# Performance work log

Measured on AMD Instinct MI355X. Metric: run time of the kernel, lower is better.

Reference implementation:

```python
import jax, jax.numpy as jnp
import numpy as np

GROUP = 32          # microscale group size for both acts and weights
FP8_MAX = 448.0     # float8_e4m3fn max
FP4_TABLE = jnp.array([0.0, 0.5, 1.0, 1.5, 2.0, 3.0, 4.0, 6.0,
                       -0.0, -0.5, -1.0, -1.5, -2.0, -3.0, -4.0, -6.0], dtype=jnp.float32)


def _ue8m0_to_float(sf):
    # uint8 exponent byte placed directly into the fp32 exponent field: 2^(e-127)
    return jax.lax.bitcast_convert_type(sf.astype(jnp.uint32) << 23, jnp.float32)


def _dequant_mxfp4(w_packed, sf):
    # w_packed: [..., K//2] ints in [0,256), two e2m1 nibbles per byte (low nibble = even elem)
    lo = FP4_TABLE[w_packed & 0xF]
    hi = FP4_TABLE[(w_packed >> 4) & 0xF]
    w = jnp.stack([lo, hi], axis=-1).reshape(*w_packed.shape[:-1], -1)   # [..., K]
    s = _ue8m0_to_float(sf)                                              # [..., K//32]
    w = w.reshape(*sf.shape, GROUP) * s[..., None]
    return w.reshape(*w_packed.shape[:-1], 2 * w_packed.shape[-1])


def _quant_dequant_fp8(x):
    # Faithful to _deepseek_v4_stage_mega_moe_inputs_kernel: per-32-group amax,
    # scale = amax/448 rounded UP to a power of two (UE8M0), cast to fp8 e4m3.
    T, D = x.shape
    xg = x.reshape(T, D // GROUP, GROUP)
    amax = jnp.maximum(jnp.max(jnp.abs(xg), axis=-1), 1e-4)
    scale = amax / FP8_MAX
    bits = jax.lax.bitcast_convert_type(scale, jnp.uint32)
    exp = ((bits >> 23) & 0xFF) + ((bits & 0x7FFFFF) != 0).astype(jnp.uint32)
    exp = jnp.clip(exp, 1, 254)
    rscale = jax.lax.bitcast_convert_type(exp << 23, jnp.float32)
    q = (xg * (1.0 / rscale)[..., None]).astype(jnp.float8_e4m3fn)
    return (q.astype(jnp.float32) * rscale[..., None]).reshape(T, D)


def setup_inputs() -> dict:
    key = jax.random.key(0)
    ks = jax.random.split(key, 7)
    T, D, I, E, K = 512, 2048, 768, 16, 8
    hidden_states = jax.random.normal(ks[0], (T, D), dtype=jnp.float32)
    topk_weights = jax.random.uniform(ks[1], (T, K), dtype=jnp.float32)
    topk_weights = topk_weights / jnp.sum(topk_weights, axis=-1, keepdims=True)
    topk_ids = jax.random.randint(ks[2], (T, K), 0, E, dtype=jnp.int32)
    w13_weight = jax.random.randint(ks[3], (E, 2 * I, D // 2), 0, 256, dtype=jnp.int32)
    w13_weight_scale = jax.random.randint(ks[4], (E, 2 * I, D // GROUP), 120, 128, dtype=jnp.int32)
    w2_weight = jax.random.randint(ks[5], (E, D, I // 2), 0, 256, dtype=jnp.int32)
    w2_weight_scale = jax.random.randint(ks[6], (E, D, I // GROUP), 120, 128, dtype=jnp.int32)
    return {"hidden_states": hidden_states, "topk_weights": topk_weights,
            "topk_ids": topk_ids, "w13_weight": w13_weight,
            "w13_weight_scale": w13_weight_scale, "w2_weight": w2_weight,
            "w2_weight_scale": w2_weight_scale}


def reference(hidden_states, topk_weights, topk_ids, w13_weight, w13_weight_scale,
              w2_weight, w2_weight_scale):
    E = w13_weight.shape[0]
    I = w13_weight.shape[1] // 2
    x = _quant_dequant_fp8(hidden_states)                 # [T, D] fp8-quantized acts
    w13 = _dequant_mxfp4(w13_weight, w13_weight_scale)    # [E, 2I, D]
    w2 = _dequant_mxfp4(w2_weight, w2_weight_scale)       # [E, D, I]
    onehot = (topk_ids[:, :, None] == jnp.arange(E)[None, None, :]).astype(jnp.float32)  # [T,K,E]
    routed = jnp.any(onehot > 0, axis=1)                  # [T, E]
    Xe = routed.T[:, :, None].astype(x.dtype) * x[None]   # [E, T, D]
    h = jnp.einsum('etd,efd->etf', Xe, w13)               # [E, T, 2I]
    gate, up = h[..., :I], h[..., I:]
    a = jax.nn.silu(gate) * up                            # SiluAndMul
    ye = jnp.einsum('eti,edi->etd', a, w2)                # [E, T, D]
    comb = jnp.einsum('tke,tk->te', onehot, topk_weights) # [T, E] routing weights
    return jnp.einsum('te,etd->td', comb, ye)             # [T, D]
```

## Files before the change

### kernel.cpp

```cpp
#include <hip/hip_runtime.h>
#include <stdint.h>
#include <math.h>

#define T_TOK 512
#define DDIM  2048
#define IDIM  768
#define NEXP  16
#define TOPK  8
#define LDB   72

typedef __attribute__((ext_vector_type(8))) short bf16x8;
typedef __attribute__((ext_vector_type(4))) float f32x4;

__device__ __forceinline__ float e4m3_rtne(float f) {
  uint32_t u = __float_as_uint(f);
  uint32_t sign = u & 0x80000000u;
  uint32_t a = u & 0x7FFFFFFFu;
  float fa = __uint_as_float(a);
  float out;
  if (fa >= 0.015625f) {
    uint32_t lsb = (a >> 20) & 1u;
    a += 0x0007FFFFu + lsb;
    a &= 0xFFF00000u;
    out = __uint_as_float(a);
  } else {
    out = rintf(fa * 512.0f) * 0.001953125f;
  }
  return __uint_as_float(__float_as_uint(out) | sign);
}

__global__ void qdq_kernel(const float* __restrict__ x, ushort* __restrict__ xq) {
  int idx = blockIdx.x * 256 + threadIdx.x;
  float v = x[idx];
  float a = fabsf(v);
#pragma unroll
  for (int m = 16; m >= 1; m >>= 1)
    a = fmaxf(a, __shfl_xor(a, m, 32));
  a = fmaxf(a, 1e-4f);
  float scale = a / 448.0f;
  uint32_t b = __float_as_uint(scale);
  uint32_t ex = ((b >> 23) & 255u) + ((b & 0x7FFFFFu) ? 1u : 0u);
  ex = ex < 1u ? 1u : (ex > 254u ? 254u : ex);
  float rscale = __uint_as_float(ex << 23);
  float inv = 1.0f / rscale;
  float r = e4m3_rtne(v * inv) * rscale;
  xq[idx] = (ushort)(__float_as_uint(r) >> 16);
}

__global__ void route_kernel(const int* __restrict__ ids, const float* __restrict__ wts,
                             int* counts, int* offsets, int* lists, float* combs,
                             int* tpe, int* tps, int* tpn) {
  int t = threadIdx.x;
  int  myid[TOPK];
  float myw[TOPK];
#pragma unroll
  for (int k = 0; k < TOPK; k++) { myid[k] = ids[t*TOPK+k]; myw[k] = wts[t*TOPK+k]; }
  int np = 0;
  for (int e = 0; e < NEXP; e++) {
    float s = 0.f; bool r = false;
#pragma unroll
    for (int k = 0; k < TOPK; k++) if (myid[k] == e) { s += myw[k]; r = true; }
    if (r) {
      int slot = atomicAdd(&counts[e], 1);
      lists[(e<<9) + slot] = t;
      combs[(e<<9) + slot] = s;
      tpe[t*TOPK + np] = e;
      tps[t*TOPK + np] = slot;
      np++;
    }
  }
  tpn[t] = np;
  __syncthreads();
  if (t == 0) {
    int acc = 0;
    for (int e = 0; e < NEXP; e++) {
      offsets[e] = acc;
      acc += atomicAdd(&counts[e], 0);
    }
    offsets[NEXP] = acc;
  }
}

__device__ __forceinline__ uint32_t dec2(uint32_t w8, uint32_t S) {
  uint32_t lo = w8 & 15u, hi = (w8 >> 4) & 15u;
  uint32_t mlo = lo & 7u, mhi = hi & 7u;
  uint32_t clo = (mlo < 2u) ? 0u : mlo;
  uint32_t chi = (mhi < 2u) ? 0u : mhi;
  uint32_t blo = (mlo == 0u) ? 0u : ((S + clo) << 6);
  uint32_t bhi = (mhi == 0u) ? 0u : ((S + chi) << 6);
  blo |= (lo & 8u) << 12;
  bhi |= (hi & 8u) << 12;
  return blo | (bhi << 16);
}

__global__ __launch_bounds__(128,2) void gemm1_kernel(
    const ushort* __restrict__ xq, const int* __restrict__ w13,
    const int* __restrict__ w13s, const int* __restrict__ counts,
    const int* __restrict__ offsets, const int* __restrict__ lists,
    const float* __restrict__ combs, ushort* __restrict__ a_buf)
{
  const int e  = blockIdx.x;
  const int i0 = blockIdx.y << 5;
  const int m0 = blockIdx.z << 7;
  const int cnt = counts[e];
  if (m0 >= cnt) return;

  __shared__ __align__(16) ushort Bsh[64*LDB];
  __shared__ int   toks[128];
  __shared__ float cmbs[128];

  const int tid = threadIdx.x;
  { int m = m0 + tid; bool v = m < cnt;
    toks[tid] = v ? lists[(e<<9)+m] : 0;
    cmbs[tid] = v ? combs[(e<<9)+m] : 0.f; }
  __syncthreads();

  const int wv = tid >> 6, l = tid & 63, l16 = l & 15, q = l >> 4;

  const ushort* arow[4];
#pragma unroll
  for (int i = 0; i < 4; i++) {
    int row = wv*64 + i*16 + l16;
    arow[i] = xq + (size_t)toks[row]*DDIM + q*8;
  }

  const int rb = tid >> 1, hb = tid & 1;
  const int feat = (rb < 32) ? (i0 + rb) : (IDIM + i0 + (rb - 32));
  const int* wrow = w13 + ((size_t)e*(2*IDIM) + feat)*(DDIM/2) + hb*16;
  const int* srow = w13s + ((size_t)e*(2*IDIM) + feat)*(DDIM/32);
  ushort* bdst = Bsh + rb*LDB + hb*32;

  f32x4 acc[4][4];
#pragma unroll
  for (int i = 0; i < 4; i++)
#pragma unroll
    for (int j = 0; j < 4; j++) acc[i][j] = (f32x4){0.f,0.f,0.f,0.f};

  for (int k0 = 0; k0 < DDIM; k0 += 64) {
    int4 wq[4];
    const int4* bp = (const int4*)(wrow + (k0 >> 1));
#pragma unroll
    for (int c = 0; c < 4; c++) wq[c] = bp[c];
    uint32_t S = (((uint32_t)srow[(k0 >> 5) + hb]) - 1u) << 1;

    bf16x8 afr[4][2];
#pragma unroll
    for (int i = 0; i < 4; i++)
#pragma unroll
      for (int s = 0; s < 2; s++)
        afr[i][s] = *(const bf16x8*)(arow[i] + k0 + s*32);

    __syncthreads();
    {
      uint32_t od[16];
      const int* wi = (const int*)wq;
#pragma unroll
      for (int c = 0; c < 16; c++) od[c] = dec2((uint32_t)wi[c], S);
#pragma unroll
      for (int c = 0; c < 4; c++)
        *(uint4*)(bdst + c*8) = make_uint4(od[4*c], od[4*c+1], od[4*c+2], od[4*c+3]);
    }
    __syncthreads();

#pragma unroll
    for (int s = 0; s < 2; s++) {
      bf16x8 bfr[4];
#pragma unroll
      for (int j = 0; j < 4; j++)
        bfr[j] = *(const bf16x8*)(Bsh + (j*16 + l16)*LDB + s*32 + q*8);
#pragma unroll
      for (int i = 0; i < 4; i++)
#pragma unroll
        for (int j = 0; j < 4; j++)
          acc[i][j] = __builtin_amdgcn_mfma_f32_16x16x32_bf16(afr[i][s], bfr[j], acc[i][j], 0, 0, 0);
    }
  }

  const int obase = offsets[e];
#pragma unroll
  for (int i = 0; i < 4; i++) {
#pragma unroll
    for (int r = 0; r < 4; r++) {
      int mrow = wv*64 + i*16 + q*4 + r;
      int gm = m0 + mrow;
      if (gm < cnt) {
        float c = cmbs[mrow];
        ushort* dst = a_buf + (size_t)(obase + gm)*IDIM + i0 + l16;
#pragma unroll
        for (int jj = 0; jj < 2; jj++) {
          float g = acc[i][jj][r], u = acc[i][jj+2][r];
          float val = (g / (1.f + expf(-g))) * u * c;
          uint32_t bb = __float_as_uint(val);
          bb += 0x7FFFu + ((bb >> 16) & 1u);
          dst[jj*16] = (ushort)(bb >> 16);
        }
      }
    }
  }
}

__global__ __launch_bounds__(128,2) void gemm2_kernel(
    const ushort* __restrict__ a_buf, const int* __restrict__ w2,
    const int* __restrict__ w2s, const int* __restrict__ counts,
    const int* __restrict__ offsets, const int* __restrict__ lists,
    float* __restrict__ out, float* __restrict__ ye, int use_ye)
{
  const int e  = blockIdx.x;
  const int n0 = blockIdx.y << 6;
  const int m0 = blockIdx.z << 7;
  const int cnt = counts[e];
  if (m0 >= cnt) return;

  __shared__ __align__(16) ushort Bsh[64*LDB];
  __shared__ int toks[128];

  const int tid = threadIdx.x;
  { int m = m0 + tid; toks[tid] = (m < cnt) ? lists[(e<<9)+m] : -1; }
  __syncthreads();

  const int wv = tid >> 6, l = tid & 63, l16 = l & 15, q = l >> 4;
  const int obase = offsets[e];

  const ushort* arow[4];
#pragma unroll
  for (int i = 0; i < 4; i++) {
    int gm = m0 + wv*64 + i*16 + l16;
    int rowc = (gm < cnt) ? gm : 0;
    arow[i] = a_buf + (size_t)(obase + rowc)*IDIM + q*8;
  }

  const int rb = tid >> 1, hb = tid & 1;
  const int* wrow = w2 + ((size_t)e*DDIM + n0 + rb)*(IDIM/2) + hb*16;
  const int* srow = w2s + ((size_t)e*DDIM + n0 + rb)*(IDIM/32);
  ushort* bdst = Bsh + rb*LDB + hb*32;

  f32x4 acc[4][4];
#pragma unroll
  for (int i = 0; i < 4; i++)
#pragma unroll
    for (int j = 0; j < 4; j++) acc[i][j] = (f32x4){0.f,0.f,0.f,0.f};

  for (int k0 = 0; k0 < IDIM; k0 += 64) {
    int4 wq[4];
    const int4* bp = (const int4*)(wrow + (k0 >> 1));
#pragma unroll
    for (int c = 0; c < 4; c++) wq[c] = bp[c];
    uint32_t S = (((uint32_t)srow[(k0 >> 5) + hb]) - 1u) << 1;

    bf16x8 afr[4][2];
#pragma unroll
    for (int i = 0; i < 4; i++)
#pragma unroll
      for (int s = 0; s < 2; s++)
        afr[i][s] = *(const bf16x8*)(arow[i] + k0 + s*32);

    __syncthreads();
    {
      uint32_t od[16];
      const int* wi = (const int*)wq;
#pragma unroll
      for (int c = 0; c < 16; c++) od[c] = dec2((uint32_t)wi[c], S);
#pragma unroll
      for (int c = 0; c < 4; c++)
        *(uint4*)(bdst + c*8) = make_uint4(od[4*c], od[4*c+1], od[4*c+2], od[4*c+3]);
    }
    __syncthreads();

#pragma unroll
    for (int s = 0; s < 2; s++) {
      bf16x8 bfr[4];
#pragma unroll
      for (int j = 0; j < 4; j++)
        bfr[j] = *(const bf16x8*)(Bsh + (j*16 + l16)*LDB + s*32 + q*8);
#pragma unroll
      for (int i = 0; i < 4; i++)
#pragma unroll
        for (int j = 0; j < 4; j++)
          acc[i][j] = __builtin_amdgcn_mfma_f32_16x16x32_bf16(afr[i][s], bfr[j], acc[i][j], 0, 0, 0);
    }
  }

#pragma unroll
  for (int i = 0; i < 4; i++) {
#pragma unroll
    for (int r = 0; r < 4; r++) {
      int mrow = wv*64 + i*16 + q*4 + r;
      int gm = m0 + mrow;
      if (gm < cnt) {
        if (use_ye) {
          float* dst = ye + (size_t)(obase + gm)*DDIM + n0 + l16;
#pragma unroll
          for (int j = 0; j < 4; j++) dst[j*16] = acc[i][j][r];
        } else {
          int tok = toks[mrow];
          float* dst = out + (size_t)tok*DDIM + n0 + l16;
#pragma unroll
          for (int j = 0; j < 4; j++) atomicAdd(&dst[j*16], acc[i][j][r]);
        }
      }
    }
  }
}

__global__ void combine_kernel(const float* __restrict__ ye, const int* __restrict__ offsets,
                               const int* __restrict__ tpe, const int* __restrict__ tps,
                               const int* __restrict__ tpn, float* __restrict__ out) {
  int t = blockIdx.x;
  int np = tpn[t];
  int rows[TOPK];
#pragma unroll
  for (int j = 0; j < TOPK; j++)
    rows[j] = (j < np) ? (offsets[tpe[t*TOPK+j]] + tps[t*TOPK+j]) : -1;
  for (int c = threadIdx.x; c < DDIM; c += 256) {
    float s = 0.f;
#pragma unroll
    for (int j = 0; j < TOPK; j++)
      if (rows[j] >= 0) s += ye[(size_t)rows[j]*DDIM + c];
    out[(size_t)t*DDIM + c] = s;
  }
}

extern "C" void kernel_launch(void* const* d_in, const int* in_sizes, int n_in,
                              void* d_out, int out_size, void* d_ws, size_t ws_size,
                              hipStream_t stream)
{
  const float* x    = (const float*)d_in[0];
  const float* tw   = (const float*)d_in[1];
  const int*   tids = (const int*)d_in[2];
  const int*   w13  = (const int*)d_in[3];
  const int*   w13s = (const int*)d_in[4];
  const int*   w2   = (const int*)d_in[5];
  const int*   w2s  = (const int*)d_in[6];
  float* out = (float*)d_out;

  char* ws = (char*)d_ws;
  size_t off = 0;
  auto alloc = [&](size_t bytes) { void* p = ws + off; off = (off + bytes + 255) & ~(size_t)255; return p; };
  ushort* xq     = (ushort*)alloc((size_t)T_TOK*DDIM*2);
  int*   counts  = (int*)alloc(64*4);
  int*   offsets = (int*)alloc(64*4);
  int*   lists   = (int*)alloc((size_t)NEXP*T_TOK*4);
  float* combs   = (float*)alloc((size_t)NEXP*T_TOK*4);
  int*   tpe     = (int*)alloc((size_t)T_TOK*TOPK*4);
  int*   tps     = (int*)alloc((size_t)T_TOK*TOPK*4);
  int*   tpn     = (int*)alloc((size_t)T_TOK*4);
  ushort* a_buf  = (ushort*)alloc((size_t)T_TOK*TOPK*IDIM*2);
  float* ye      = (float*)(ws + off);
  size_t need_ye = off + (size_t)T_TOK*TOPK*DDIM*4;
  int use_ye = (ws_size >= need_ye) ? 1 : 0;

  hipMemsetAsync(counts, 0, 256, stream);
  hipMemsetAsync(out, 0, (size_t)out_size * 4, stream);

  qdq_kernel<<<(T_TOK*DDIM)/256, 256, 0, stream>>>(x, xq);
  route_kernel<<<1, T_TOK, 0, stream>>>(tids, tw, counts, offsets, lists, combs, tpe, tps, tpn);
  gemm1_kernel<<<dim3(NEXP, IDIM/32, 4), 128, 0, stream>>>(
      xq, w13, w13s, counts, offsets, lists, combs, a_buf);
  gemm2_kernel<<<dim3(NEXP, DDIM/64, 4), 128, 0, stream>>>(
      a_buf, w2, w2s, counts, offsets, lists, out, ye, use_ye);
  if (use_ye)
    combine_kernel<<<T_TOK, 256, 0, stream>>>(ye, offsets, tpe, tps, tpn, out);
}
```

Before: 335.5 us.

## Double-buffer dequantized weight tiles, widen blocks to 256 threads, store ye as bf16

Both GEMM kernels now use 256 threads with four waves, each wave covering 32 rows instead of 64, and double-buffered shared-memory weight tiles. The next tile's weights and activations are prefetched and decoded while MFMAs run on the current buffer, which leaves one barrier per k-step. The per-expert intermediate ye is now stored as bf16 instead of fp32, halving its write and read traffic in gemm2 and the combine kernel. This costs extra rounding in the expert outputs, more shared memory, and more registers per thread for the prefetched data.

After: 315.0 us. 1.06x faster.

```diff
diff --git a/kernel.cpp b/kernel.cpp
--- a/kernel.cpp
+++ b/kernel.cpp
@@ -93,7 +93,7 @@
   return blo | (bhi << 16);
 }
 
-__global__ __launch_bounds__(128,2) void gemm1_kernel(
+__global__ __launch_bounds__(256,3) void gemm1_kernel(
     const ushort* __restrict__ xq, const int* __restrict__ w13,
     const int* __restrict__ w13s, const int* __restrict__ counts,
     const int* __restrict__ offsets, const int* __restrict__ lists,
@@ -105,83 +105,111 @@
   const int cnt = counts[e];
   if (m0 >= cnt) return;
 
-  __shared__ __align__(16) ushort Bsh[64*LDB];
+  __shared__ __align__(16) ushort Bsh[2][64*LDB];
   __shared__ int   toks[128];
   __shared__ float cmbs[128];
 
   const int tid = threadIdx.x;
-  { int m = m0 + tid; bool v = m < cnt;
+  if (tid < 128) {
+    int m = m0 + tid; bool v = m < cnt;
     toks[tid] = v ? lists[(e<<9)+m] : 0;
-    cmbs[tid] = v ? combs[(e<<9)+m] : 0.f; }
+    cmbs[tid] = v ? combs[(e<<9)+m] : 0.f;
+  }
   __syncthreads();
 
   const int wv = tid >> 6, l = tid & 63, l16 = l & 15, q = l >> 4;
 
-  const ushort* arow[4];
-#pragma unroll
-  for (int i = 0; i < 4; i++) {
-    int row = wv*64 + i*16 + l16;
-    arow[i] = xq + (size_t)toks[row]*DDIM + q*8;
-  }
-
-  const int rb = tid >> 1, hb = tid & 1;
+  const ushort* arow[2];
+#pragma unroll
+  for (int i = 0; i < 2; i++)
+    arow[i] = xq + (size_t)toks[wv*32 + i*16 + l16]*DDIM + q*8;
+
+  const int rb = tid >> 2, hq = tid & 3;
   const int feat = (rb < 32) ? (i0 + rb) : (IDIM + i0 + (rb - 32));
-  const int* wrow = w13 + ((size_t)e*(2*IDIM) + feat)*(DDIM/2) + hb*16;
-  const int* srow = w13s + ((size_t)e*(2*IDIM) + feat)*(DDIM/32);
-  ushort* bdst = Bsh + rb*LDB + hb*32;
-
-  f32x4 acc[4][4];
-#pragma unroll
-  for (int i = 0; i < 4; i++)
+  const int* wrow = w13 + ((size_t)e*(2*IDIM) + feat)*(DDIM/2) + hq*8;
+  const int* srow = w13s + ((size_t)e*(2*IDIM) + feat)*(DDIM/32) + (hq >> 1);
+  const int bdst = rb*LDB + hq*16;
+
+  f32x4 acc[2][4];
+#pragma unroll
+  for (int i = 0; i < 2; i++)
 #pragma unroll
     for (int j = 0; j < 4; j++) acc[i][j] = (f32x4){0.f,0.f,0.f,0.f};
 
+  bf16x8 afr[2][2];
+#pragma unroll
+  for (int i = 0; i < 2; i++)
+#pragma unroll
+    for (int s = 0; s < 2; s++)
+      afr[i][s] = *(const bf16x8*)(arow[i] + s*32);
+  {
+    int4 w0 = *(const int4*)(wrow);
+    int4 w1 = *(const int4*)(wrow + 4);
+    uint32_t S = (((uint32_t)srow[0]) - 1u) << 1;
+    int wi[8] = {w0.x,w0.y,w0.z,w0.w, w1.x,w1.y,w1.z,w1.w};
+    uint32_t od[8];
+#pragma unroll
+    for (int c = 0; c < 8; c++) od[c] = dec2((uint32_t)wi[c], S);
+    ushort* d = &Bsh[0][bdst];
+    *(uint4*)d       = make_uint4(od[0], od[1], od[2], od[3]);
+    *(uint4*)(d + 8) = make_uint4(od[4], od[5], od[6], od[7]);
+  }
+  __syncthreads();
+
   for (int k0 = 0; k0 < DDIM; k0 += 64) {
-    int4 wq[4];
-    const int4* bp = (const int4*)(wrow + (k0 >> 1));
-#pragma unroll
-    for (int c = 0; c < 4; c++) wq[c] = bp[c];
-    uint32_t S = (((uint32_t)srow[(k0 >> 5) + hb]) - 1u) << 1;
-
-    bf16x8 afr[4][2];
-#pragma unroll
-    for (int i = 0; i < 4; i++)
-#pragma unroll
-      for (int s = 0; s < 2; s++)
-        afr[i][s] = *(const bf16x8*)(arow[i] + k0 + s*32);
-
-    __syncthreads();
-    {
-      uint32_t od[16];
-      const int* wi = (const int*)wq;
-#pragma unroll
-      for (int c = 0; c < 16; c++) od[c] = dec2((uint32_t)wi[c], S);
-#pragma unroll
-      for (int c = 0; c < 4; c++)
-        *(uint4*)(bdst + c*8) = make_uint4(od[4*c], od[4*c+1], od[4*c+2], od[4*c+3]);
-    }
-    __syncthreads();
+    const int cur = (k0 >> 6) & 1;
+    const bool more = (k0 + 64) < DDIM;
+
+    int4 nw0, nw1; uint32_t nS = 0;
+    bf16x8 nafr[2][2];
+    if (more) {
+      const int* wp = wrow + ((k0 + 64) >> 1);
+      nw0 = *(const int4*)wp;
+      nw1 = *(const int4*)(wp + 4);
+      nS = (((uint32_t)srow[(k0 + 64) >> 5]) - 1u) << 1;
+#pragma unroll
+      for (int i = 0; i < 2; i++)
+#pragma unroll
+        for (int s = 0; s < 2; s++)
+          nafr[i][s] = *(const bf16x8*)(arow[i] + k0 + 64 + s*32);
+    }
 
 #pragma unroll
     for (int s = 0; s < 2; s++) {
       bf16x8 bfr[4];
 #pragma unroll
       for (int j = 0; j < 4; j++)
-        bfr[j] = *(const bf16x8*)(Bsh + (j*16 + l16)*LDB + s*32 + q*8);
-#pragma unroll
-      for (int i = 0; i < 4; i++)
+        bfr[j] = *(const bf16x8*)&Bsh[cur][(j*16 + l16)*LDB + s*32 + q*8];
+#pragma unroll
+      for (int i = 0; i < 2; i++)
 #pragma unroll
         for (int j = 0; j < 4; j++)
           acc[i][j] = __builtin_amdgcn_mfma_f32_16x16x32_bf16(afr[i][s], bfr[j], acc[i][j], 0, 0, 0);
     }
+
+    if (more) {
+      int wi[8] = {nw0.x,nw0.y,nw0.z,nw0.w, nw1.x,nw1.y,nw1.z,nw1.w};
+      uint32_t od[8];
+#pragma unroll
+      for (int c = 0; c < 8; c++) od[c] = dec2((uint32_t)wi[c], nS);
+      ushort* d = &Bsh[1 - cur][bdst];
+      *(uint4*)d       = make_uint4(od[0], od[1], od[2], od[3]);
+      *(uint4*)(d + 8) = make_uint4(od[4], od[5], od[6], od[7]);
+#pragma unroll
+      for (int i = 0; i < 2; i++)
+#pragma unroll
+        for (int s = 0; s < 2; s++)
+          afr[i][s] = nafr[i][s];
+    }
+    __syncthreads();
   }
 
   const int obase = offsets[e];
 #pragma unroll
-  for (int i = 0; i < 4; i++) {
+  for (int i = 0; i < 2; i++) {
 #pragma unroll
     for (int r = 0; r < 4; r++) {
-      int mrow = wv*64 + i*16 + q*4 + r;
+      int mrow = wv*32 + i*16 + q*4 + r;
       int gm = m0 + mrow;
       if (gm < cnt) {
         float c = cmbs[mrow];
@@ -199,11 +227,11 @@
   }
 }
 
-__global__ __launch_bounds__(128,2) void gemm2_kernel(
+__global__ __launch_bounds__(256,3) void gemm2_kernel(
     const ushort* __restrict__ a_buf, const int* __restrict__ w2,
     const int* __restrict__ w2s, const int* __restrict__ counts,
     const int* __restrict__ offsets, const int* __restrict__ lists,
-    float* __restrict__ out, float* __restrict__ ye, int use_ye)
+    float* __restrict__ out, ushort* __restrict__ ye, int use_ye)
 {
   const int e  = blockIdx.x;
   const int n0 = blockIdx.y << 6;
@@ -211,86 +239,121 @@
   const int cnt = counts[e];
   if (m0 >= cnt) return;
 
-  __shared__ __align__(16) ushort Bsh[64*LDB];
+  __shared__ __align__(16) ushort Bsh[2][64*LDB];
   __shared__ int toks[128];
 
   const int tid = threadIdx.x;
-  { int m = m0 + tid; toks[tid] = (m < cnt) ? lists[(e<<9)+m] : -1; }
+  if (tid < 128) {
+    int m = m0 + tid;
+    toks[tid] = (m < cnt) ? lists[(e<<9)+m] : -1;
+  }
   __syncthreads();
 
   const int wv = tid >> 6, l = tid & 63, l16 = l & 15, q = l >> 4;
   const int obase = offsets[e];
 
-  const ushort* arow[4];
-#pragma unroll
-  for (int i = 0; i < 4; i++) {
-    int gm = m0 + wv*64 + i*16 + l16;
+  const ushort* arow[2];
+#pragma unroll
+  for (int i = 0; i < 2; i++) {
+    int gm = m0 + wv*32 + i*16 + l16;
     int rowc = (gm < cnt) ? gm : 0;
     arow[i] = a_buf + (size_t)(obase + rowc)*IDIM + q*8;
   }
 
-  const int rb = tid >> 1, hb = tid & 1;
-  const int* wrow = w2 + ((size_t)e*DDIM + n0 + rb)*(IDIM/2) + hb*16;
-  const int* srow = w2s + ((size_t)e*DDIM + n0 + rb)*(IDIM/32);
-  ushort* bdst = Bsh + rb*LDB + hb*32;
-
-  f32x4 acc[4][4];
-#pragma unroll
-  for (int i = 0; i < 4; i++)
+  const int rb = tid >> 2, hq = tid & 3;
+  const int* wrow = w2 + ((size_t)e*DDIM + n0 + rb)*(IDIM/2) + hq*8;
+  const int* srow = w2s + ((size_t)e*DDIM + n0 + rb)*(IDIM/32) + (hq >> 1);
+  const int bdst = rb*LDB + hq*16;
+
+  f32x4 acc[2][4];
+#pragma unroll
+  for (int i = 0; i < 2; i++)
 #pragma unroll
     for (int j = 0; j < 4; j++) acc[i][j] = (f32x4){0.f,0.f,0.f,0.f};
 
+  bf16x8 afr[2][2];
+#pragma unroll
+  for (int i = 0; i < 2; i++)
+#pragma unroll
+    for (int s = 0; s < 2; s++)
+      afr[i][s] = *(const bf16x8*)(arow[i] + s*32);
+  {
+    int4 w0 = *(const int4*)(wrow);
+    int4 w1 = *(const int4*)(wrow + 4);
+    uint32_t S = (((uint32_t)srow[0]) - 1u) << 1;
+    int wi[8] = {w0.x,w0.y,w0.z,w0.w, w1.x,w1.y,w1.z,w1.w};
+    uint32_t od[8];
+#pragma unroll
+    for (int c = 0; c < 8; c++) od[c] = dec2((uint32_t)wi[c], S);
+    ushort* d = &Bsh[0][bdst];
+    *(uint4*)d       = make_uint4(od[0], od[1], od[2], od[3]);
+    *(uint4*)(d + 8) = make_uint4(od[4], od[5], od[6], od[7]);
+  }
+  __syncthreads();
+
   for (int k0 = 0; k0 < IDIM; k0 += 64) {
-    int4 wq[4];
-    const int4* bp = (const int4*)(wrow + (k0 >> 1));
-#pragma unroll
-    for (int c = 0; c < 4; c++) wq[c] = bp[c];
-    uint32_t S = (((uint32_t)srow[(k0 >> 5) + hb]) - 1u) << 1;
-
-    bf16x8 afr[4][2];
-#pragma unroll
-    for (int i = 0; i < 4; i++)
-#pragma unroll
-      for (int s = 0; s < 2; s++)
-        afr[i][s] = *(const bf16x8*)(arow[i] + k0 + s*32);
-
-    __syncthreads();
-    {
-      uint32_t od[16];
-      const int* wi = (const int*)wq;
-#pragma unroll
-      for (int c = 0; c < 16; c++) od[c] = dec2((uint32_t)wi[c], S);
-#pragma unroll
-      for (int c = 0; c < 4; c++)
-        *(uint4*)(bdst + c*8) = make_uint4(od[4*c], od[4*c+1], od[4*c+2], od[4*c+3]);
-    }
-    __syncthreads();
+    const int cur = (k0 >> 6) & 1;
+    const bool more = (k0 + 64) < IDIM;
+
+    int4 nw0, nw1; uint32_t nS = 0;
+    bf16x8 nafr[2][2];
+    if (more) {
+      const int* wp = wrow + ((k0 + 64) >> 1);
+      nw0 = *(const int4*)wp;
+      nw1 = *(const int4*)(wp + 4);
+      nS = (((uint32_t)srow[(k0 + 64) >> 5]) - 1u) << 1;
+#pragma unroll
+      for (int i = 0; i < 2; i++)
+#pragma unroll
+        for (int s = 0; s < 2; s++)
+          nafr[i][s] = *(const bf16x8*)(arow[i] + k0 + 64 + s*32);
+    }
 
 #pragma unroll
     for (int s = 0; s < 2; s++) {
       bf16x8 bfr[4];
 #pragma unroll
       for (int j = 0; j < 4; j++)
-        bfr[j] = *(const bf16x8*)(Bsh + (j*16 + l16)*LDB + s*32 + q*8);
-#pragma unroll
-      for (int i = 0; i < 4; i++)
+        bfr[j] = *(const bf16x8*)&Bsh[cur][(j*16 + l16)*LDB + s*32 + q*8];
+#pragma unroll
+      for (int i = 0; i < 2; i++)
 #pragma unroll
         for (int j = 0; j < 4; j++)
           acc[i][j] = __builtin_amdgcn_mfma_f32_16x16x32_bf16(afr[i][s], bfr[j], acc[i][j], 0, 0, 0);
     }
-  }
-
-#pragma unroll
-  for (int i = 0; i < 4; i++) {
+
+    if (more) {
+      int wi[8] = {nw0.x,nw0.y,nw0.z,nw0.w, nw1.x,nw1.y,nw1.z,nw1.w};
+      uint32_t od[8];
+#pragma unroll
+      for (int c = 0; c < 8; c++) od[c] = dec2((uint32_t)wi[c], nS);
+      ushort* d = &Bsh[1 - cur][bdst];
+      *(uint4*)d       = make_uint4(od[0], od[1], od[2], od[3]);
+      *(uint4*)(d + 8) = make_uint4(od[4], od[5], od[6], od[7]);
+#pragma unroll
+      for (int i = 0; i < 2; i++)
+#pragma unroll
+        for (int s = 0; s < 2; s++)
+          afr[i][s] = nafr[i][s];
+    }
+    __syncthreads();
+  }
+
+#pragma unroll
+  for (int i = 0; i < 2; i++) {
 #pragma unroll
     for (int r = 0; r < 4; r++) {
-      int mrow = wv*64 + i*16 + q*4 + r;
+      int mrow = wv*32 + i*16 + q*4 + r;
       int gm = m0 + mrow;
       if (gm < cnt) {
         if (use_ye) {
-          float* dst = ye + (size_t)(obase + gm)*DDIM + n0 + l16;
-#pragma unroll
-          for (int j = 0; j < 4; j++) dst[j*16] = acc[i][j][r];
+          ushort* dst = ye + (size_t)(obase + gm)*DDIM + n0 + l16;
+#pragma unroll
+          for (int j = 0; j < 4; j++) {
+            uint32_t bb = __float_as_uint(acc[i][j][r]);
+            bb += 0x7FFFu + ((bb >> 16) & 1u);
+            dst[j*16] = (ushort)(bb >> 16);
+          }
         } else {
           int tok = toks[mrow];
           float* dst = out + (size_t)tok*DDIM + n0 + l16;
@@ -302,7 +365,7 @@
   }
 }
 
-__global__ void combine_kernel(const float* __restrict__ ye, const int* __restrict__ offsets,
+__global__ void combine_kernel(const ushort* __restrict__ ye, const int* __restrict__ offsets,
                                const int* __restrict__ tpe, const int* __restrict__ tps,
                                const int* __restrict__ tpn, float* __restrict__ out) {
   int t = blockIdx.x;
@@ -315,7 +378,8 @@
     float s = 0.f;
 #pragma unroll
     for (int j = 0; j < TOPK; j++)
-      if (rows[j] >= 0) s += ye[(size_t)rows[j]*DDIM + c];
+      if (rows[j] >= 0)
+        s += __uint_as_float(((uint32_t)ye[(size_t)rows[j]*DDIM + c]) << 16);
     out[(size_t)t*DDIM + c] = s;
   }
 }
@@ -345,8 +409,8 @@
   int*   tps     = (int*)alloc((size_t)T_TOK*TOPK*4);
   int*   tpn     = (int*)alloc((size_t)T_TOK*4);
   ushort* a_buf  = (ushort*)alloc((size_t)T_TOK*TOPK*IDIM*2);
-  float* ye      = (float*)(ws + off);
-  size_t need_ye = off + (size_t)T_TOK*TOPK*DDIM*4;
+  ushort* ye     = (ushort*)(ws + off);
+  size_t need_ye = off + (size_t)T_TOK*TOPK*DDIM*2;
   int use_ye = (ws_size >= need_ye) ? 1 : 0;
 
   hipMemsetAsync(counts, 0, 256, stream);
@@ -354,9 +418,9 @@
 
   qdq_kernel<<<(T_TOK*DDIM)/256, 256, 0, stream>>>(x, xq);
   route_kernel<<<1, T_TOK, 0, stream>>>(tids, tw, counts, offsets, lists, combs, tpe, tps, tpn);
-  gemm1_kernel<<<dim3(NEXP, IDIM/32, 4), 128, 0, stream>>>(
+  gemm1_kernel<<<dim3(NEXP, IDIM/32, 4), 256, 0, stream>>>(
       xq, w13, w13s, counts, offsets, lists, combs, a_buf);
-  gemm2_kernel<<<dim3(NEXP, DDIM/64, 4), 128, 0, stream>>>(
+  gemm2_kernel<<<dim3(NEXP, DDIM/64, 4), 256, 0, stream>>>(
       a_buf, w2, w2s, counts, offsets, lists, out, ye, use_ye);
   if (use_ye)
     combine_kernel<<<T_TOK, 256, 0, stream>>>(ye, offsets, tpe, tps, tpn, out);
```
